# Kernel tuning notes

Hardware: AMD Instinct MI355X
Metric: run time of the kernel (lower is better)

Reference implementation:

```python
import jax, jax.numpy as jnp
import numpy as np

N_AUTHOR, N_PAPER = 20000, 40000
E = 400000
IN_DIM, HIDDEN, HEADS, NUM_CLASSES, NUM_LAYERS = 128, 128, 8, 16, 2
DIM = HIDDEN // HEADS
NEG_SLOPE = 0.2
AUTHOR_RAW = 64


def setup_inputs() -> dict:
    key = jax.random.key(0)
    ks = jax.random.split(key, 16)
    s = 0.05
    return {
        'x_author': jax.random.normal(ks[0], (N_AUTHOR, AUTHOR_RAW), jnp.float32),
        'x_paper': jax.random.normal(ks[1], (N_PAPER, IN_DIM), jnp.float32),
        'Wa': jax.random.normal(ks[2], (AUTHOR_RAW, IN_DIM), jnp.float32) * s,
        'proj_w': jax.random.normal(ks[3], (NUM_LAYERS, 2, IN_DIM, HIDDEN), jnp.float32) * s,
        'proj_b': jnp.zeros((NUM_LAYERS, 2, HIDDEN), jnp.float32),
        'att_src': jax.random.normal(ks[4], (NUM_LAYERS, 3, HEADS, DIM), jnp.float32) * s,
        'att_dst': jax.random.normal(ks[5], (NUM_LAYERS, 3, HEADS, DIM), jnp.float32) * s,
        'klin_w': jax.random.normal(ks[6], (NUM_LAYERS, HIDDEN, HIDDEN), jnp.float32) * s,
        'klin_b': jnp.zeros((NUM_LAYERS, HIDDEN), jnp.float32),
        'q': jax.random.normal(ks[7], (NUM_LAYERS, HIDDEN), jnp.float32) * s,
        'lin_w': jax.random.normal(ks[8], (HIDDEN, NUM_CLASSES), jnp.float32) * s,
        'lin_b': jnp.zeros((NUM_CLASSES,), jnp.float32),
        'ei_writes': jnp.stack([jax.random.randint(ks[9], (E,), 0, N_AUTHOR),
                                jax.random.randint(ks[10], (E,), 0, N_PAPER)]),
        'ei_written_by': jnp.stack([jax.random.randint(ks[11], (E,), 0, N_PAPER),
                                    jax.random.randint(ks[12], (E,), 0, N_AUTHOR)]),
        'ei_cites': jnp.stack([jax.random.randint(ks[13], (E,), 0, N_PAPER),
                               jax.random.randint(ks[14], (E,), 0, N_PAPER)]),
    }


def _segment_softmax(scores, seg, num_segments):
    # scores: [E, H]; softmax over edges sharing a destination node.
    m = jax.ops.segment_max(scores, seg, num_segments=num_segments)
    m = jnp.where(jnp.isfinite(m), m, 0.0)
    e = jnp.exp(scores - m[seg])
    denom = jax.ops.segment_sum(e, seg, num_segments=num_segments)
    return e / (denom[seg] + 1e-16)


def _han_forward(x_author, x_paper, Wa, proj_w, proj_b, att_src, att_dst,
                 klin_w, klin_b, q, lin_w, lin_b,
                 ei_writes, ei_written_by, ei_cites):
    # Type-alignment projector (author: 64 -> 128, no bias; paper: Identity)
    x = {'author': x_author @ Wa, 'paper': x_paper}
    nsize = {'author': N_AUTHOR, 'paper': N_PAPER}
    ntidx = {'author': 0, 'paper': 1}
    edge_types = [('author', 'paper', ei_writes),
                  ('paper', 'author', ei_written_by),
                  ('paper', 'paper', ei_cites)]
    for l in range(NUM_LAYERS):
        # Per-node-type projection -> [N, H, D]
        xh = {nt: (x[nt] @ proj_w[l, ntidx[nt]] + proj_b[l, ntidx[nt]]).reshape(-1, HEADS, DIM)
              for nt in x}
        outs = {'author': [], 'paper': []}
        for e_id, (src, dst, ei) in enumerate(edge_types):
            a_src = (xh[src] * att_src[l, e_id]).sum(-1)  # [N_src, H]
            a_dst = (xh[dst] * att_dst[l, e_id]).sum(-1)  # [N_dst, H]
            si, di = ei[0], ei[1]
            alpha = a_src[si] + a_dst[di]                 # [E, H]
            alpha = jnp.where(alpha >= 0, alpha, NEG_SLOPE * alpha)  # leaky_relu
            alpha = _segment_softmax(alpha, di, nsize[dst])
            # attention dropout omitted (eval mode)
            msg = (xh[src][si] * alpha[:, :, None]).reshape(-1, HIDDEN)  # [E, HIDDEN]
            agg = jax.ops.segment_sum(msg, di, num_segments=nsize[dst])
            outs[dst].append(jax.nn.relu(agg))
        # Semantic-level attention over metapath embeddings per node type
        newx = {}
        for nt, xs in outs.items():
            stk = jnp.stack(xs)  # [M, N, F]
            score = (q[l] * jnp.tanh(stk @ klin_w[l] + klin_b[l]).mean(axis=1)).sum(-1)  # [M]
            attn = jax.nn.softmax(score)
            newx[nt] = (attn[:, None, None] * stk).sum(0)
        x = newx
        if l < NUM_LAYERS - 1:
            x = {nt: jax.nn.relu(v) for nt, v in x.items()}
            # feature dropout omitted (eval mode)
    return x['paper'] @ lin_w + lin_b  # [N_PAPER, NUM_CLASSES]


def reference(x_author, x_paper, Wa, proj_w, proj_b, att_src, att_dst,
              klin_w, klin_b, q, lin_w, lin_b,
              ei_writes, ei_written_by, ei_cites):
    return _han_forward(x_author, x_paper, Wa, proj_w, proj_b, att_src, att_dst,
                        klin_w, klin_b, q, lin_w, lin_b,
                        ei_writes, ei_written_by, ei_cites)
```

## Files before the change

### kernel.cpp

```cpp
#include <hip/hip_runtime.h>
#include <hip/hip_bf16.h>

typedef __hip_bfloat16 bf16;
typedef __hip_bfloat162 bf162;

#define N_AUTHOR 20000
#define N_PAPER  40000
#define NEDGE    400000
#define HID      128
#define HEADS    8
#define DIMH     16
#define NCLS     16

typedef short short8v __attribute__((ext_vector_type(8)));
typedef float f32x4   __attribute__((ext_vector_type(4)));

__device__ __forceinline__ float b2f(short s){
    return __uint_as_float(((unsigned)(unsigned short)s) << 16);
}
__device__ __forceinline__ short f2bs(float v){
    unsigned u = __float_as_uint(v);
    unsigned r = (u + 0x7FFFu + ((u >> 16) & 1u)) >> 16;
    return (short)r;
}
__device__ __forceinline__ float fastrcp(float x){ return __builtin_amdgcn_rcpf(x); }

__device__ __forceinline__ float fast_tanh(float x){
    x = fminf(fmaxf(x, -15.f), 15.f);
    float e = __expf(2.f * x);
    return 1.f - 2.f * fastrcp(e + 1.f);
}

template<int KDIM, int EPI, int BLEND, int AF32>
__device__ __forceinline__ void bgemm_body(
    const void* __restrict__ Av, const bf16* __restrict__ A2, float w0, float w1,
    const bf16* __restrict__ Wt, const float* __restrict__ Bb,
    bf16* __restrict__ C, const float* __restrict__ qv, float* __restrict__ score,
    int M, int brow, float* red)
{
    const int tid  = threadIdx.x;
    const int lane = tid & 63;
    const int wv   = tid >> 6;
    const int lr   = lane & 15;
    const int quad = lane >> 4;
    const int row0 = brow * 64 + wv * 16;
    const int arow_i = row0 + lr;
    const bool rowok = arow_i < M;

    short8v afrag[KDIM / 32];
    if (AF32) {
        const float* arow = (const float*)Av + (long)arow_i * KDIM;
        #pragma unroll
        for (int kc = 0; kc < KDIM / 32; kc++) {
            short8v f = {0,0,0,0,0,0,0,0};
            if (rowok) {
                float4 v0 = *(const float4*)(arow + kc * 32 + quad * 8);
                float4 v1 = *(const float4*)(arow + kc * 32 + quad * 8 + 4);
                f[0] = f2bs(v0.x); f[1] = f2bs(v0.y); f[2] = f2bs(v0.z); f[3] = f2bs(v0.w);
                f[4] = f2bs(v1.x); f[5] = f2bs(v1.y); f[6] = f2bs(v1.z); f[7] = f2bs(v1.w);
            }
            afrag[kc] = f;
        }
    } else {
        const bf16* arow  = (const bf16*)Av + (long)arow_i * KDIM;
        const bf16* arow2 = BLEND ? (A2 + (long)arow_i * KDIM) : nullptr;
        #pragma unroll
        for (int kc = 0; kc < KDIM / 32; kc++) {
            short8v f = {0,0,0,0,0,0,0,0};
            if (rowok) {
                f = *(const short8v*)(arow + kc * 32 + quad * 8);
                if (BLEND) {
                    short8v g = *(const short8v*)(arow2 + kc * 32 + quad * 8);
                    #pragma unroll
                    for (int j = 0; j < 8; j++)
                        f[j] = f2bs(w0 * b2f(f[j]) + w1 * b2f(g[j]));
                }
            }
            afrag[kc] = f;
        }
    }

    f32x4 acc[8];
    #pragma unroll
    for (int ct = 0; ct < 8; ct++) acc[ct] = (f32x4){0.f, 0.f, 0.f, 0.f};

    #pragma unroll
    for (int k0 = 0; k0 < KDIM / 32; k0 += 2) {
        short8v bf[2][8];
        #pragma unroll
        for (int u = 0; u < 2; u++)
            #pragma unroll
            for (int ct = 0; ct < 8; ct++)
                bf[u][ct] = *(const short8v*)(Wt + (long)(ct * 16 + lr) * KDIM + (k0 + u) * 32 + quad * 8);
        #pragma unroll
        for (int u = 0; u < 2; u++)
            #pragma unroll
            for (int ct = 0; ct < 8; ct++)
                acc[ct] = __builtin_amdgcn_mfma_f32_16x16x32_bf16(afrag[k0 + u], bf[u][ct], acc[ct], 0, 0, 0);
    }

    if (EPI == 0) {
        #pragma unroll
        for (int ct = 0; ct < 8; ct++) {
            float bc = Bb ? Bb[ct * 16 + lr] : 0.f;
            #pragma unroll
            for (int r = 0; r < 4; r++) {
                int orow = row0 + quad * 4 + r;
                if (orow < M)
                    C[(long)orow * HID + ct * 16 + lr] = __float2bfloat16(acc[ct][r] + bc);
            }
        }
    } else {
        float part = 0.f;
        #pragma unroll
        for (int ct = 0; ct < 8; ct++) {
            float bc = Bb ? Bb[ct * 16 + lr] : 0.f;
            float qc = qv[ct * 16 + lr];
            #pragma unroll
            for (int r = 0; r < 4; r++) {
                int orow = row0 + quad * 4 + r;
                if (orow < M) part += qc * fast_tanh(acc[ct][r] + bc);
            }
        }
        red[tid] = part;
        __syncthreads();
        for (int s = 128; s > 0; s >>= 1) {
            if (tid < s) red[tid] += red[tid + s];
            __syncthreads();
        }
        if (tid == 0) atomicAdd(score, red[0]);
    }
}

template<int KDIM, int EPI, int B1>
__global__ __launch_bounds__(256) void bgemm_pair_kernel(
    const bf16* __restrict__ A0, const bf16* __restrict__ Wt0, const float* __restrict__ Bb0,
    bf16* __restrict__ C0, float* __restrict__ score0, int M0, int NB0,
    const bf16* __restrict__ A1, const bf16* __restrict__ A1b, const float* __restrict__ scw,
    const bf16* __restrict__ Wt1, const float* __restrict__ Bb1,
    bf16* __restrict__ C1, float* __restrict__ score1, int M1,
    const float* __restrict__ qv)
{
    __shared__ float red[256];
    const int bx = blockIdx.x;
    if (bx < NB0) {
        bgemm_body<KDIM, EPI, 0, 0>(A0, nullptr, 0.f, 0.f, Wt0, Bb0, C0, qv, score0, M0, bx, red);
    } else {
        float w0 = 0.f, w1 = 0.f;
        if (B1) {
            float s0 = scw[0] * (1.f / N_PAPER);
            float s1 = scw[1] * (1.f / N_PAPER);
            float m = fmaxf(s0, s1);
            float e0 = __expf(s0 - m), e1 = __expf(s1 - m);
            float inv = fastrcp(e0 + e1);
            w0 = e0 * inv; w1 = e1 * inv;
        }
        bgemm_body<KDIM, EPI, B1, 0>(A1, A1b, w0, w1, Wt1, Bb1, C1, qv, score1, M1, bx - NB0, red);
    }
}

#define R_WA  (128 * 64)
#define R_PW  (4 * 128 * 128)
#define R_KW  (2 * 128 * 128)
#define CONV_W_TOT (R_WA + R_PW + R_KW)

#define CNT_OFF1 N_PAPER
#define CNT_OFF2 (N_PAPER + N_AUTHOR)
#define NDEST    (2 * N_PAPER + N_AUTHOR)
#define NCOPY 8
#define CW    2
#define CIDX(c, d) (((c) * NDEST + (d)) * CW)
#define CNT_TOT (NCOPY * NDEST * CW)
#define E3 (3 * NEDGE)
#define HU 16
#define HIST_TT (E3 / HU)

__global__ __launch_bounds__(256) void convw_kernel(
    const float* __restrict__ Wa, const float* __restrict__ proj_w,
    const float* __restrict__ klin_w,
    bf16* __restrict__ wt_wa, bf16* __restrict__ wt_proj, bf16* __restrict__ wt_klin)
{
    int i = blockIdx.x * 256 + threadIdx.x;
    if (i >= CONV_W_TOT) return;
    if (i < R_WA) {
        int n = i >> 6, k = i & 63;
        wt_wa[i] = __float2bfloat16(Wa[k * 128 + n]);
    } else if (i < R_WA + R_PW) {
        int j = i - R_WA;
        int m = j >> 14, r = j & 16383;
        int n = r >> 7, k = r & 127;
        wt_proj[j] = __float2bfloat16(proj_w[m * 16384 + k * 128 + n]);
    } else {
        int j = i - R_WA - R_PW;
        int m = j >> 14, r = j & 16383;
        int n = r >> 7, k = r & 127;
        wt_klin[j] = __float2bfloat16(klin_w[m * 16384 + k * 128 + n]);
    }
}

__global__ __launch_bounds__(256) void hist_gemm_kernel(
    const int* __restrict__ d0, const int* __restrict__ d1, const int* __restrict__ d2,
    int* __restrict__ cnt, unsigned short* __restrict__ rank, int HB,
    const float* __restrict__ xa_f, const bf16* __restrict__ wt_wa, bf16* __restrict__ buf_a, int GA64,
    const float* __restrict__ xp_f, const bf16* __restrict__ pw_p, const float* __restrict__ pb_p,
    bf16* __restrict__ xh_p)
{
    __shared__ float red[256];
    int bx = blockIdx.x;
    if (bx < HB) {
        int c = bx & (NCOPY - 1);
        int* mycnt = cnt + c * NDEST * CW;
        int t = bx * 256 + threadIdx.x;
        if (t >= HIST_TT) return;
        #pragma unroll
        for (int u = 0; u < HU; u++) {
            int i = t + u * HIST_TT;
            int r;
            if (i < NEDGE)            r = atomicAdd(&mycnt[d0[i] * CW], 1);
            else if (i < 2*NEDGE)     r = atomicAdd(&mycnt[(CNT_OFF1 + d1[i - NEDGE]) * CW], 1);
            else                      r = atomicAdd(&mycnt[(CNT_OFF2 + d2[i - 2*NEDGE]) * CW], 1);
            rank[i] = (unsigned short)((c << 13) | r);
        }
        return;
    }
    bx -= HB;
    if (bx < GA64) {
        bgemm_body<64, 0, 0, 1>(xa_f, nullptr, 0.f, 0.f, wt_wa, nullptr, buf_a,
                                nullptr, nullptr, N_AUTHOR, bx, red);
        return;
    }
    bx -= GA64;
    bgemm_body<128, 0, 0, 1>(xp_f, nullptr, 0.f, 0.f, pw_p, pb_p, xh_p,
                             nullptr, nullptr, N_PAPER, bx, red);
}

__device__ __forceinline__ int job_nd(int j){ return j == 1 ? N_AUTHOR : N_PAPER; }
__device__ __forceinline__ int job_off(int j){ return j == 0 ? 0 : (j == 1 ? CNT_OFF1 : CNT_OFF2); }

__global__ __launch_bounds__(256) void scan_a3_kernel(const int* __restrict__ cnt,
                                                      int* __restrict__ bsum)
{
    int j = blockIdx.y;
    int nd = job_nd(j), off = job_off(j);
    __shared__ int s[256];
    int tid = threadIdx.x;
    int i = blockIdx.x * 256 + tid;
    int v = 0;
    if (i < nd) {
        #pragma unroll
        for (int c = 0; c < NCOPY; c++) v += cnt[CIDX(c, off + i)];
    }
    s[tid] = v;
    __syncthreads();
    for (int st = 128; st > 0; st >>= 1) {
        if (tid < st) s[tid] += s[tid + st];
        __syncthreads();
    }
    if (tid == 0) bsum[j * 256 + blockIdx.x] = s[0];
}

__global__ __launch_bounds__(256) void scan_bc_kernel(int* __restrict__ cnt,
    const int* __restrict__ bsum,
    int* __restrict__ roff0, int* __restrict__ roff1, int* __restrict__ roff2)
{
    int j = blockIdx.y;
    int nd = job_nd(j), off = job_off(j);
    int* roff = j == 0 ? roff0 : (j == 1 ? roff1 : roff2);
    __shared__ int sb[256];
    __shared__ int s[256];
    int tid = threadIdx.x;
    int bx = blockIdx.x;
    int nb = (nd + 255) / 256;
    int bvt = (tid < nb) ? bsum[j * 256 + tid] : 0;
    sb[tid] = bvt;
    __syncthreads();
    for (int o = 1; o < 256; o <<= 1) {
        int t = (tid >= o) ? sb[tid - o] : 0;
        __syncthreads();
        sb[tid] += t;
        __syncthreads();
    }
    int base0 = sb[bx] - bsum[j * 256 + bx];
    int i = bx * 256 + tid;
    int cc[NCOPY];
    int v = 0;
    if (i < nd) {
        #pragma unroll
        for (int c = 0; c < NCOPY; c++) { cc[c] = cnt[CIDX(c, off + i)]; v += cc[c]; }
    }
    s[tid] = v;
    __syncthreads();
    for (int o = 1; o < 256; o <<= 1) {
        int t = (tid >= o) ? s[tid - o] : 0;
        __syncthreads();
        s[tid] += t;
        __syncthreads();
    }
    if (i < nd) {
        int base = base0 + s[tid] - v;
        roff[i] = base;
        #pragma unroll
        for (int c = 0; c < NCOPY; c++) { cnt[CIDX(c, off + i)] = base; base += cc[c]; }
    }
    if (bx == 0 && tid == 0) roff[nd] = NEDGE;
}

__global__ __launch_bounds__(256) void fill_natt_kernel(
    const int* __restrict__ s0, const int* __restrict__ d0,
    const int* __restrict__ s1, const int* __restrict__ d1,
    const int* __restrict__ s2, const int* __restrict__ d2,
    const int* __restrict__ cnt, const unsigned short* __restrict__ rank,
    unsigned short* __restrict__ c0, unsigned short* __restrict__ c1, unsigned short* __restrict__ c2,
    int HB,
    const bf16* __restrict__ A, const bf16* __restrict__ Wt, const float* __restrict__ Bb,
    bf16* __restrict__ C, int GAb,
    const bf16* __restrict__ xh_p,
    const float* __restrict__ ad0v, const float* __restrict__ as1v,
    const float* __restrict__ as2v, const float* __restrict__ ad2v,
    float* __restrict__ o_e0d, float* __restrict__ o_e1s,
    float* __restrict__ o_e2s, float* __restrict__ o_e2d)
{
    __shared__ float red[256];
    int bx = blockIdx.x;
    if (bx < HB) {
        int t = bx * 256 + threadIdx.x;
        if (t >= HIST_TT) return;
        #pragma unroll
        for (int u = 0; u < HU; u++) {
            int i = t + u * HIST_TT;
            int rw = rank[i];
            int c = rw >> 13, rk = rw & 0x1FFF;
            if (i < NEDGE) {
                int d = d0[i];
                c0[cnt[CIDX(c, d)] + rk] = (unsigned short)s0[i];
            } else if (i < 2*NEDGE) {
                int e = i - NEDGE, d = d1[e];
                c1[cnt[CIDX(c, CNT_OFF1 + d)] + rk] = (unsigned short)s1[e];
            } else {
                int e = i - 2*NEDGE, d = d2[e];
                c2[cnt[CIDX(c, CNT_OFF2 + d)] + rk] = (unsigned short)s2[e];
            }
        }
        return;
    }
    bx -= HB;
    if (bx < GAb) {
        bgemm_body<128, 0, 0, 0>(A, nullptr, 0.f, 0.f, Wt, Bb, C,
                                 nullptr, nullptr, N_AUTHOR, bx, red);
        return;
    }
    bx -= GAb;
    int i = bx * 256 + threadIdx.x;
    if (i >= N_PAPER * HEADS) return;
    int n = i >> 3, h = i & 7;
    const bf16* row = xh_p + (long)n * HID + h * DIMH;
    float x[DIMH];
    #pragma unroll
    for (int d = 0; d < DIMH; d++) x[d] = __bfloat162float(row[d]);
    float sA = 0.f, sB = 0.f, sC = 0.f, sD = 0.f;
    #pragma unroll
    for (int d = 0; d < DIMH; d++) {
        sA += x[d] * ad0v[h*DIMH + d];
        sB += x[d] * as1v[h*DIMH + d];
        sC += x[d] * as2v[h*DIMH + d];
        sD += x[d] * ad2v[h*DIMH + d];
    }
    o_e0d[i] = sA; o_e1s[i] = sB; o_e2s[i] = sC; o_e2d[i] = sD;
}

__global__ void node_att_multi_kernel(const bf16* __restrict__ xh,
    const float* __restrict__ A0, const float* __restrict__ A1,
    float* __restrict__ O0, float* __restrict__ O1, int N)
{
    int i = blockIdx.x * blockDim.x + threadIdx.x;
    if (i >= N * HEADS) return;
    int n = i >> 3, h = i & 7;
    const bf16* row = xh + (long)n * HID + h * DIMH;
    float x[DIMH];
    #pragma unroll
    for (int d = 0; d < DIMH; d++) x[d] = __bfloat162float(row[d]);
    if (A0) { float s = 0.f;
        #pragma unroll
        for (int d = 0; d < DIMH; d++) s += x[d] * A0[h*DIMH + d];
        O0[i] = s; }
    if (A1) { float s = 0.f;
        #pragma unroll
        for (int d = 0; d < DIMH; d++) s += x[d] * A1[h*DIMH + d];
        O1[i] = s; }
}

__global__ __launch_bounds__(256) void natt_l1_kernel(
    const bf16* __restrict__ xh_a, const float* __restrict__ as0, float* __restrict__ a_e0s, int AB,
    const bf16* __restrict__ xh_p, const float* __restrict__ ad0,
    const float* __restrict__ as2, const float* __restrict__ ad2,
    float* __restrict__ a_e0d, float* __restrict__ a_e2s, float* __restrict__ a_e2d)
{
    int bx = blockIdx.x, tid = threadIdx.x;
    if (bx < AB) {
        int i = bx * 256 + tid;
        if (i >= N_AUTHOR * HEADS) return;
        int n = i >> 3, h = i & 7;
        const bf16* row = xh_a + (long)n * HID + h * DIMH;
        float s = 0.f;
        #pragma unroll
        for (int d = 0; d < DIMH; d++) s += __bfloat162float(row[d]) * as0[h*DIMH + d];
        a_e0s[i] = s;
        return;
    }
    int i = (bx - AB) * 256 + tid;
    if (i >= N_PAPER * HEADS) return;
    int n = i >> 3, h = i & 7;
    const bf16* row = xh_p + (long)n * HID + h * DIMH;
    float x[DIMH];
    #pragma unroll
    for (int d = 0; d < DIMH; d++) x[d] = __bfloat162float(row[d]);
    float sA = 0.f, sC = 0.f, sD = 0.f;
    #pragma unroll
    for (int d = 0; d < DIMH; d++) {
        sA += x[d] * ad0[h*DIMH + d];
        sC += x[d] * as2[h*DIMH + d];
        sD += x[d] * ad2[h*DIMH + d];
    }
    a_e0d[i] = sA; a_e2s[i] = sC; a_e2d[i] = sD;
}

template<int U>
__device__ __forceinline__ void gather1_dev(int bid,
    const int* __restrict__ roff, const unsigned short* __restrict__ csrc,
    const float* __restrict__ as_, const float* __restrict__ ad_,
    const bf16* __restrict__ xh, bf16* __restrict__ out, int Ndst)
{
    int lane = threadIdx.x & 63;
    int li   = lane & 15;
    int sub  = lane >> 4;
    int w = bid * 16 + (threadIdx.x >> 6) * 4 + sub;
    if (w >= Ndst) return;
    int h = li >> 1;
    int beg = roff[w], n = roff[w + 1] - beg;
    float adv = ad_[(long)w * 8 + h];
    float den = 0.f;
    float acc[8];
    #pragma unroll
    for (int j = 0; j < 8; j++) acc[j] = 0.f;
    int cm = n > 0 ? n - 1 : 0;
    for (int i = 0; i < n; i += U) {
        int s[U];
        #pragma unroll
        for (int u = 0; u < U; u++) s[u] = csrc[beg + min(i + u, cm)];
        float av[U]; short8v xv[U];
        #pragma unroll
        for (int u = 0; u < U; u++) {
            av[u] = as_[(long)s[u] * 8 + h];
            xv[u] = *(const short8v*)(xh + (long)s[u] * HID + li * 8);
        }
        #pragma unroll
        for (int u = 0; u < U; u++) {
            float a = av[u] + adv;
            a = a >= 0.f ? a : 0.2f * a;
            float wt = __expf(fminf(a, 60.f));
            wt = (i + u < n) ? wt : 0.f;
            den += wt;
            #pragma unroll
            for (int j = 0; j < 8; j++)
                acc[j] = fmaf(b2f(xv[u][j]), wt, acc[j]);
        }
    }
    float inv = fastrcp(den + 1e-16f);
    short8v o;
    #pragma unroll
    for (int j = 0; j < 8; j++) o[j] = f2bs(fmaxf(acc[j] * inv, 0.f));
    *(short8v*)(out + (long)w * HID + li * 8) = o;
}

__global__ __launch_bounds__(256) void gather_split_kernel(
    const int* __restrict__ roff0, const unsigned short* __restrict__ csrc0,
    const float* __restrict__ as0, const float* __restrict__ ad0,
    const bf16* __restrict__ xha, bf16* __restrict__ out0,
    const int* __restrict__ roff2, const unsigned short* __restrict__ csrc2,
    const float* __restrict__ as2, const float* __restrict__ ad2,
    const bf16* __restrict__ xhp, bf16* __restrict__ out2,
    int PB,
    const int* __restrict__ roff1, const unsigned short* __restrict__ csrc1,
    const float* __restrict__ as1, const float* __restrict__ ad1,
    bf16* __restrict__ out_a)
{
    int bx = blockIdx.x;
    if (bx < PB) {
        gather1_dev<8>(bx, roff0, csrc0, as0, ad0, xha, out0, N_PAPER);
        return;
    }
    bx -= PB;
    if (bx < PB) {
        gather1_dev<8>(bx, roff2, csrc2, as2, ad2, xhp, out2, N_PAPER);
        return;
    }
    bx -= PB;
    gather1_dev<8>(bx, roff1, csrc1, as1, ad1, xhp, out_a, N_AUTHOR);
}

__global__ __launch_bounds__(256) void final_lin_fused_kernel(
    const bf16* __restrict__ a0, const bf16* __restrict__ a1,
    const float* __restrict__ score,
    const float* __restrict__ W, const float* __restrict__ B, float* __restrict__ out)
{
    __shared__ float Ws[HID * NCLS];
    int tid = threadIdx.x;
    for (int i = tid; i < HID * NCLS; i += 256) Ws[i] = W[i];
    __syncthreads();
    float s0 = score[0] * (1.f / N_PAPER);
    float s1 = score[1] * (1.f / N_PAPER);
    float m = fmaxf(s0, s1);
    float e0 = __expf(s0 - m), e1 = __expf(s1 - m);
    float inv = 1.f / (e0 + e1);
    float w0 = e0 * inv, w1 = e1 * inv;
    int i = blockIdx.x * 256 + tid;
    if (i >= N_PAPER * NCLS) return;
    int n = i >> 4, c = i & 15;
    float acc = B[c];
    const bf16* x0 = a0 + (long)n * HID;
    const bf16* x1 = a1 + (long)n * HID;
    #pragma unroll 16
    for (int k = 0; k < HID; k++)
        acc = fmaf(fmaf(w0, __bfloat162float(x0[k]), w1 * __bfloat162float(x1[k])),
                   Ws[k * NCLS + c], acc);
    out[i] = acc;
}

extern "C" void kernel_launch(void* const* d_in, const int* in_sizes, int n_in,
                              void* d_out, int out_size, void* d_ws, size_t ws_size,
                              hipStream_t stream)
{
    const float* x_author = (const float*)d_in[0];
    const float* x_paper  = (const float*)d_in[1];
    const float* Wa       = (const float*)d_in[2];
    const float* proj_w   = (const float*)d_in[3];
    const float* proj_b   = (const float*)d_in[4];
    const float* att_src  = (const float*)d_in[5];
    const float* att_dst  = (const float*)d_in[6];
    const float* klin_w   = (const float*)d_in[7];
    const float* klin_b   = (const float*)d_in[8];
    const float* qv       = (const float*)d_in[9];
    const float* lin_w    = (const float*)d_in[10];
    const float* lin_b    = (const float*)d_in[11];
    const int*  ei_w      = (const int*)d_in[12];
    const int*  ei_wb     = (const int*)d_in[13];
    const int*  ei_c      = (const int*)d_in[14];
    float* out = (float*)d_out;
    (void)ws_size; (void)in_sizes; (void)n_in; (void)out_size;

    char* base = (char*)d_ws;
    size_t off = 0;
    auto alloc = [&](size_t bytes) {
        void* p = base + off;
        off = (off + bytes + 255) & ~(size_t)255;
        return p;
    };
    bf16*  xh_a  = (bf16*) alloc((size_t)N_AUTHOR * HID * 2);
    bf16*  xh_p  = (bf16*) alloc((size_t)N_PAPER  * HID * 2);
    bf16*  buf_a = (bf16*) alloc((size_t)N_AUTHOR * HID * 2);
    bf16*  buf_p = (bf16*) alloc((size_t)N_PAPER  * HID * 2);
    bf16*  agg_p1= (bf16*) alloc((size_t)N_PAPER  * HID * 2);
    bf16*  wt_wa   = (bf16*)alloc((size_t)R_WA * 2);
    bf16*  wt_proj = (bf16*)alloc((size_t)R_PW * 2);
    bf16*  wt_klin = (bf16*)alloc((size_t)R_KW * 2);
    float* a_e0s = (float*)alloc((size_t)N_AUTHOR * HEADS * 4);
    float* a_e0d = (float*)alloc((size_t)N_PAPER  * HEADS * 4);
    float* a_e1s = (float*)alloc((size_t)N_PAPER  * HEADS * 4);
    float* a_e1d = (float*)alloc((size_t)N_AUTHOR * HEADS * 4);
    float* a_e2s = (float*)alloc((size_t)N_PAPER  * HEADS * 4);
    float* a_e2d = (float*)alloc((size_t)N_PAPER  * HEADS * 4);
    float* score  = (float*)alloc(64);
    int* roff0 = (int*)alloc((size_t)(N_PAPER  + 1) * 4);
    int* roff1 = (int*)alloc((size_t)(N_AUTHOR + 1) * 4);
    int* roff2 = (int*)alloc((size_t)(N_PAPER  + 1) * 4);
    unsigned short* csrc0 = (unsigned short*)alloc((size_t)NEDGE * 2 + 64);
    unsigned short* csrc1 = (unsigned short*)alloc((size_t)NEDGE * 2 + 64);
    unsigned short* csrc2 = (unsigned short*)alloc((size_t)NEDGE * 2 + 64);
    int* cnt   = (int*)alloc((size_t)CNT_TOT * 4);
    unsigned short* rank = (unsigned short*)alloc((size_t)E3 * 2);
    int* bsum  = (int*)alloc(3 * 256 * 4);

    const int GA = (N_AUTHOR + 63) / 64;
    const int GP = (N_PAPER  + 63) / 64;
    const int NBMAX = (N_PAPER + 255) / 256;
    const int HB = (HIST_TT + 255) / 256;
    const int CONVB = (CONV_W_TOT + 255) / 256;
    const int NATTP = (N_PAPER * HEADS + 255) / 256;
    const int NATTA = (N_AUTHOR * HEADS + 255) / 256;
    const int PGB = (N_PAPER + 15) / 16;
    const int AGB = (N_AUTHOR + 15) / 16;

    hipMemsetAsync(cnt, 0, (size_t)CNT_TOT * 4, stream);
    hipMemsetAsync(score, 0, 64, stream);

    convw_kernel<<<CONVB, 256, 0, stream>>>(
        Wa, proj_w, klin_w, wt_wa, wt_proj, wt_klin);
    hist_gemm_kernel<<<HB + GA + GP, 256, 0, stream>>>(
        ei_w + NEDGE, ei_wb + NEDGE, ei_c + NEDGE, cnt, rank, HB,
        x_author, wt_wa, buf_a, GA,
        x_paper, wt_proj + (size_t)1 * HID * HID, proj_b + (size_t)1 * HID, xh_p);
    scan_a3_kernel<<<dim3(NBMAX, 3), 256, 0, stream>>>(cnt, bsum);
    scan_bc_kernel<<<dim3(NBMAX, 3), 256, 0, stream>>>(cnt, bsum, roff0, roff1, roff2);

    const float* as0_0 = att_src + 0 * HID; const float* ad0_0 = att_dst + 0 * HID;
    const float* as1_0 = att_src + 1 * HID; const float* ad1_0 = att_dst + 1 * HID;
    const float* as2_0 = att_src + 2 * HID; const float* ad2_0 = att_dst + 2 * HID;

    fill_natt_kernel<<<HB + GA + NATTP, 256, 0, stream>>>(
        ei_w, ei_w + NEDGE, ei_wb, ei_wb + NEDGE, ei_c, ei_c + NEDGE,
        cnt, rank, csrc0, csrc1, csrc2, HB,
        buf_a, wt_proj + (size_t)0 * HID * HID, proj_b + (size_t)0 * HID, xh_a, GA,
        xh_p, ad0_0, as1_0, as2_0, ad2_0,
        a_e0d, a_e1s, a_e2s, a_e2d);
    node_att_multi_kernel<<<NATTA, 256, 0, stream>>>(
        xh_a, as0_0, ad1_0, a_e0s, a_e1d, N_AUTHOR);

    gather_split_kernel<<<2 * PGB + AGB, 256, 0, stream>>>(
        roff0, csrc0, a_e0s, a_e0d, xh_a, buf_p,
        roff2, csrc2, a_e2s, a_e2d, xh_p, agg_p1,
        PGB,
        roff1, csrc1, a_e1s, a_e1d, buf_a);

    bgemm_pair_kernel<128, 1, 0><<<2 * GP, 256, 0, stream>>>(
        buf_p, wt_klin, klin_b, (bf16*)nullptr, score + 0, N_PAPER, GP,
        agg_p1, nullptr, nullptr, wt_klin, klin_b, (bf16*)nullptr, score + 1, N_PAPER,
        qv);

    bgemm_pair_kernel<128, 0, 1><<<GA + GP, 256, 0, stream>>>(
        buf_a, wt_proj + (size_t)2 * HID * HID, proj_b + (size_t)2 * HID, xh_a,
        nullptr, N_AUTHOR, GA,
        buf_p, agg_p1, score,
        wt_proj + (size_t)3 * HID * HID, proj_b + (size_t)3 * HID, xh_p,
        nullptr, N_PAPER, nullptr);
    hipMemsetAsync(score, 0, 64, stream);

    const float* as0_1 = att_src + 3 * HID; const float* ad0_1 = att_dst + 3 * HID;
    const float* as2_1 = att_src + 5 * HID; const float* ad2_1 = att_dst + 5 * HID;

    natt_l1_kernel<<<NATTA + NATTP, 256, 0, stream>>>(
        xh_a, as0_1, a_e0s, NATTA,
        xh_p, ad0_1, as2_1, ad2_1, a_e0d, a_e2s, a_e2d);

    gather_split_kernel<<<2 * PGB, 256, 0, stream>>>(
        roff0, csrc0, a_e0s, a_e0d, xh_a, buf_p,
        roff2, csrc2, a_e2s, a_e2d, xh_p, agg_p1,
        PGB,
        roff1, csrc1, a_e1s, a_e1d, nullptr);

    bgemm_pair_kernel<128, 1, 0><<<2 * GP, 256, 0, stream>>>(
        buf_p, wt_klin + (size_t)HID * HID, klin_b + HID, (bf16*)nullptr, score + 0, N_PAPER, GP,
        agg_p1, nullptr, nullptr, wt_klin + (size_t)HID * HID, klin_b + HID,
        (bf16*)nullptr, score + 1, N_PAPER,
        qv + HID);

    final_lin_fused_kernel<<<(N_PAPER * NCLS + 255) / 256, 256, 0, stream>>>(
        buf_p, agg_p1, score, lin_w, lin_b, out);
}
```

Baseline: 397.1 us.

## Split gather by feature slices and store attention scores head-major

Attention score arrays move from node-major [N,8] to head-major [8,N] layout. The gather kernel now splits each destination's 128 features into four 32-feature slices handled by separate blocks, with four lanes per destination and 16 destinations per wave, and the unroll drops from 8 to 4. Interleaving the slice index in the block index is meant to let co-scheduled blocks share cached source rows while each reads a narrower span, raising parallelism and the number of edge loads in flight. The cost is that index and score reads are repeated four times, and each gathered 32-feature access is a smaller transaction.

```diff
diff --git a/kernel.cpp b/kernel.cpp
--- a/kernel.cpp
+++ b/kernel.cpp
@@ -365,7 +365,8 @@
         sC += x[d] * as2v[h*DIMH + d];
         sD += x[d] * ad2v[h*DIMH + d];
     }
-    o_e0d[i] = sA; o_e1s[i] = sB; o_e2s[i] = sC; o_e2d[i] = sD;
+    long o = (long)h * N_PAPER + n;
+    o_e0d[o] = sA; o_e1s[o] = sB; o_e2s[o] = sC; o_e2d[o] = sD;
 }
 
 __global__ void node_att_multi_kernel(const bf16* __restrict__ xh,
@@ -379,14 +380,15 @@
     float x[DIMH];
     #pragma unroll
     for (int d = 0; d < DIMH; d++) x[d] = __bfloat162float(row[d]);
+    long o = (long)h * N + n;
     if (A0) { float s = 0.f;
         #pragma unroll
         for (int d = 0; d < DIMH; d++) s += x[d] * A0[h*DIMH + d];
-        O0[i] = s; }
+        O0[o] = s; }
     if (A1) { float s = 0.f;
         #pragma unroll
         for (int d = 0; d < DIMH; d++) s += x[d] * A1[h*DIMH + d];
-        O1[i] = s; }
+        O1[o] = s; }
 }
 
 __global__ __launch_bounds__(256) void natt_l1_kernel(
@@ -404,7 +406,7 @@
         float s = 0.f;
         #pragma unroll
         for (int d = 0; d < DIMH; d++) s += __bfloat162float(row[d]) * as0[h*DIMH + d];
-        a_e0s[i] = s;
+        a_e0s[(long)h * N_AUTHOR + n] = s;
         return;
     }
     int i = (bx - AB) * 256 + tid;
@@ -421,37 +423,40 @@
         sC += x[d] * as2[h*DIMH + d];
         sD += x[d] * ad2[h*DIMH + d];
     }
-    a_e0d[i] = sA; a_e2s[i] = sC; a_e2d[i] = sD;
+    long o = (long)h * N_PAPER + n;
+    a_e0d[o] = sA; a_e2s[o] = sC; a_e2d[o] = sD;
 }
 
 template<int U>
-__device__ __forceinline__ void gather1_dev(int bid,
+__device__ __forceinline__ void gatherS_dev(int dgrp, int s,
     const int* __restrict__ roff, const unsigned short* __restrict__ csrc,
-    const float* __restrict__ as_, const float* __restrict__ ad_,
-    const bf16* __restrict__ xh, bf16* __restrict__ out, int Ndst)
+    const float* __restrict__ asH, const float* __restrict__ adH,
+    int Ns, int Nd, const bf16* __restrict__ xh, bf16* __restrict__ out)
 {
     int lane = threadIdx.x & 63;
-    int li   = lane & 15;
-    int sub  = lane >> 4;
-    int w = bid * 16 + (threadIdx.x >> 6) * 4 + sub;
-    if (w >= Ndst) return;
-    int h = li >> 1;
+    int wv   = threadIdx.x >> 6;
+    int ld   = lane & 3;
+    int dw   = lane >> 2;
+    int w = dgrp * 64 + wv * 16 + dw;
+    if (w >= Nd) return;
+    int h  = 2 * s + (ld >> 1);
+    int fo = s * 32 + ld * 8;
     int beg = roff[w], n = roff[w + 1] - beg;
-    float adv = ad_[(long)w * 8 + h];
+    float adv = adH[(long)h * Nd + w];
     float den = 0.f;
     float acc[8];
     #pragma unroll
     for (int j = 0; j < 8; j++) acc[j] = 0.f;
     int cm = n > 0 ? n - 1 : 0;
     for (int i = 0; i < n; i += U) {
-        int s[U];
-        #pragma unroll
-        for (int u = 0; u < U; u++) s[u] = csrc[beg + min(i + u, cm)];
+        int sv[U];
+        #pragma unroll
+        for (int u = 0; u < U; u++) sv[u] = csrc[beg + min(i + u, cm)];
         float av[U]; short8v xv[U];
         #pragma unroll
         for (int u = 0; u < U; u++) {
-            av[u] = as_[(long)s[u] * 8 + h];
-            xv[u] = *(const short8v*)(xh + (long)s[u] * HID + li * 8);
+            av[u] = asH[(long)h * Ns + sv[u]];
+            xv[u] = *(const short8v*)(xh + (long)sv[u] * HID + fo);
         }
         #pragma unroll
         for (int u = 0; u < U; u++) {
@@ -469,33 +474,51 @@
     short8v o;
     #pragma unroll
     for (int j = 0; j < 8; j++) o[j] = f2bs(fmaxf(acc[j] * inv, 0.f));
-    *(short8v*)(out + (long)w * HID + li * 8) = o;
-}
-
-__global__ __launch_bounds__(256) void gather_split_kernel(
+    *(short8v*)(out + (long)w * HID + fo) = o;
+}
+
+__global__ __launch_bounds__(256) void gather_l0_kernel(
     const int* __restrict__ roff0, const unsigned short* __restrict__ csrc0,
     const float* __restrict__ as0, const float* __restrict__ ad0,
     const bf16* __restrict__ xha, bf16* __restrict__ out0,
     const int* __restrict__ roff2, const unsigned short* __restrict__ csrc2,
     const float* __restrict__ as2, const float* __restrict__ ad2,
-    const bf16* __restrict__ xhp, bf16* __restrict__ out2,
-    int PB,
+    const bf16* __restrict__ xhp, bf16* __restrict__ out2, int PB,
     const int* __restrict__ roff1, const unsigned short* __restrict__ csrc1,
     const float* __restrict__ as1, const float* __restrict__ ad1,
     bf16* __restrict__ out_a)
 {
-    int bx = blockIdx.x;
-    if (bx < PB) {
-        gather1_dev<8>(bx, roff0, csrc0, as0, ad0, xha, out0, N_PAPER);
-        return;
-    }
-    bx -= PB;
-    if (bx < PB) {
-        gather1_dev<8>(bx, roff2, csrc2, as2, ad2, xhp, out2, N_PAPER);
-        return;
-    }
-    bx -= PB;
-    gather1_dev<8>(bx, roff1, csrc1, as1, ad1, xhp, out_a, N_AUTHOR);
+    int s = blockIdx.x & 3;
+    int r = blockIdx.x >> 2;
+    if (r < PB) {
+        gatherS_dev<4>(r, s, roff0, csrc0, as0, ad0, N_AUTHOR, N_PAPER, xha, out0);
+        return;
+    }
+    r -= PB;
+    if (r < PB) {
+        gatherS_dev<4>(r, s, roff2, csrc2, as2, ad2, N_PAPER, N_PAPER, xhp, out2);
+        return;
+    }
+    r -= PB;
+    gatherS_dev<4>(r, s, roff1, csrc1, as1, ad1, N_PAPER, N_AUTHOR, xhp, out_a);
+}
+
+__global__ __launch_bounds__(256) void gather_l1_kernel(
+    const int* __restrict__ roff0, const unsigned short* __restrict__ csrc0,
+    const float* __restrict__ as0, const float* __restrict__ ad0,
+    const bf16* __restrict__ xha, bf16* __restrict__ out0,
+    const int* __restrict__ roff2, const unsigned short* __restrict__ csrc2,
+    const float* __restrict__ as2, const float* __restrict__ ad2,
+    const bf16* __restrict__ xhp, bf16* __restrict__ out2, int PB)
+{
+    int s = blockIdx.x & 3;
+    int r = blockIdx.x >> 2;
+    if (r < PB) {
+        gatherS_dev<4>(r, s, roff0, csrc0, as0, ad0, N_AUTHOR, N_PAPER, xha, out0);
+        return;
+    }
+    r -= PB;
+    gatherS_dev<4>(r, s, roff2, csrc2, as2, ad2, N_PAPER, N_PAPER, xhp, out2);
 }
 
 __global__ __launch_bounds__(256) void final_lin_fused_kernel(
@@ -587,8 +610,8 @@
     const int CONVB = (CONV_W_TOT + 255) / 256;
     const int NATTP = (N_PAPER * HEADS + 255) / 256;
     const int NATTA = (N_AUTHOR * HEADS + 255) / 256;
-    const int PGB = (N_PAPER + 15) / 16;
-    const int AGB = (N_AUTHOR + 15) / 16;
+    const int PGB64 = (N_PAPER + 63) / 64;
+    const int AGB64 = (N_AUTHOR + 63) / 64;
 
     hipMemsetAsync(cnt, 0, (size_t)CNT_TOT * 4, stream);
     hipMemsetAsync(score, 0, 64, stream);
@@ -615,10 +638,9 @@
     node_att_multi_kernel<<<NATTA, 256, 0, stream>>>(
         xh_a, as0_0, ad1_0, a_e0s, a_e1d, N_AUTHOR);
 
-    gather_split_kernel<<<2 * PGB + AGB, 256, 0, stream>>>(
+    gather_l0_kernel<<<4 * (2 * PGB64 + AGB64), 256, 0, stream>>>(
         roff0, csrc0, a_e0s, a_e0d, xh_a, buf_p,
-        roff2, csrc2, a_e2s, a_e2d, xh_p, agg_p1,
-        PGB,
+        roff2, csrc2, a_e2s, a_e2d, xh_p, agg_p1, PGB64,
         roff1, csrc1, a_e1s, a_e1d, buf_a);
 
     bgemm_pair_kernel<128, 1, 0><<<2 * GP, 256, 0, stream>>>(
@@ -641,11 +663,9 @@
         xh_a, as0_1, a_e0s, NATTA,
         xh_p, ad0_1, as2_1, ad2_1, a_e0d, a_e2s, a_e2d);
 
-    gather_split_kernel<<<2 * PGB, 256, 0, stream>>>(
+    gather_l1_kernel<<<4 * (2 * PGB64), 256, 0, stream>>>(
         roff0, csrc0, a_e0s, a_e0d, xh_a, buf_p,
-        roff2, csrc2, a_e2s, a_e2d, xh_p, agg_p1,
-        PGB,
-        roff1, csrc1, a_e1s, a_e1d, nullptr);
+        roff2, csrc2, a_e2s, a_e2d, xh_p, agg_p1, PGB64);
 
     bgemm_pair_kernel<128, 1, 0><<<2 * GP, 256, 0, stream>>>(
         buf_p, wt_klin + (size_t)HID * HID, klin_b + HID, (bf16*)nullptr, score + 0, N_PAPER, GP,
```

After: 462.0 us. 1.16x slower.
